# Performance work log

Hardware: AMD Instinct MI355X
Metric: run time of the kernel (lower is better)

## Reference

```python
import jax, jax.numpy as jnp
import numpy as np

N = 50000   # nodes
R = 50      # relations
B = 30      # bases
F_IN = 64   # input features
H = 64      # hidden channels
C = 8       # classes
E = 1000000 # edges


def setup_inputs() -> dict:
    key = jax.random.key(0)
    ks = jax.random.split(key, 16)
    x = jax.random.normal(ks[0], (N, F_IN), jnp.float32)
    edge_index = jax.random.randint(ks[1], (2, E), 0, N)
    edge_type = jax.random.randint(ks[2], (E,), 0, R)
    inp = {"x": x, "edge_index": edge_index, "edge_type": edge_type}
    dims = [(F_IN, H), (H, H), (H, C)]
    i = 3
    for l, (din, dout) in enumerate(dims):
        s = 1.0 / np.sqrt(din)
        inp[f"bases{l}"] = jax.random.normal(ks[i], (B, din, dout), jnp.float32) * s; i += 1
        inp[f"comp{l}"] = jax.random.normal(ks[i], (R, B), jnp.float32) / np.sqrt(B); i += 1
        inp[f"root{l}"] = jax.random.normal(ks[i], (din, dout), jnp.float32) * s; i += 1
        inp[f"bias{l}"] = jnp.zeros((dout,), jnp.float32); i += 1
    return inp


def _rgcn(x, bases, comp, root, bias, src, seg):
    # Per-relation mean aggregation (PyG RGCNConv default aggr='mean'):
    # segment id = dst * R + relation. Mean of source features per (dst, rel),
    # then basis-decomposed transform (linearity lets transform follow the mean).
    din = x.shape[1]
    sums = jax.ops.segment_sum(x[src], seg, num_segments=N * R)          # [N*R, din]
    cnt = jax.ops.segment_sum(jnp.ones((seg.shape[0],), x.dtype), seg, num_segments=N * R)
    inv = jnp.where(cnt > 0, 1.0 / jnp.maximum(cnt, 1.0), 0.0)
    agg = (sums * inv[:, None]).reshape(N, R, din)                        # [N, R, din]
    t = jnp.einsum('nri,rb->nbi', agg, comp)                              # [N, B, din]
    msg = jnp.einsum('nbi,bio->no', t, bases)                             # [N, dout]
    return msg + x @ root + bias


def reference(x, edge_index, edge_type,
              bases0, comp0, root0, bias0,
              bases1, comp1, root1, bias1,
              bases2, comp2, root2, bias2):
    src, dst = edge_index[0], edge_index[1]
    seg = dst * R + edge_type
    params = [(bases0, comp0, root0, bias0),
              (bases1, comp1, root1, bias1),
              (bases2, comp2, root2, bias2)]
    x1 = x
    for b, c, r, bi in params:
        x1 = _rgcn(x, b, c, r, bi, src, seg)
        x = jax.nn.relu(x1)
    # original returns log_softmax of the last conv's pre-ReLU output
    return jax.nn.log_softmax(x1, axis=1)
```

## Files before the change

### kernel.cpp

```cpp
#include <hip/hip_runtime.h>
#include <hip/hip_bf16.h>
#include <stdint.h>

#define NN   50000
#define RR   50
#define BB   30
#define DIN  64
#define EE   1000000
#define KTOT (BB*DIN + DIN)
#define NBW  16
#define ROWE (KTOT + 8)
#define CPAD 32

typedef __attribute__((ext_vector_type(8))) short short8;
typedef __attribute__((ext_vector_type(4))) float floatx4;

#define RFL(x) __builtin_amdgcn_readfirstlane(x)


__global__ void k_hist(const int* __restrict__ dst, const int* __restrict__ et,
                       int* __restrict__ cnt, int* __restrict__ dcount) {
    int e = blockIdx.x * 256 + threadIdx.x;
    if (e < EE) {
        int d = dst[e], r = et[e];
        atomicAdd(&cnt[d * RR + r], 1);
        atomicAdd(&dcount[d], 1);
    }
}

__global__ void k_scan1(const int* __restrict__ dcount, int* __restrict__ doff,
                        int* __restrict__ bsum) {
    __shared__ int sh[256];
    int t = threadIdx.x;
    int i = blockIdx.x * 256 + t;
    int v = (i < NN) ? dcount[i] : 0;
    sh[t] = v;
    __syncthreads();
    for (int s = 1; s < 256; s <<= 1) {
        int add = (t >= s) ? sh[t - s] : 0;
        __syncthreads();
        sh[t] += add;
        __syncthreads();
    }
    int incl = sh[t];
    if (i < NN) doff[i] = incl - v;
    if (t == 255) bsum[blockIdx.x] = incl;
}

__global__ void k_scan2(int* __restrict__ bsum, int nbv) {
    __shared__ int sh[256];
    int t = threadIdx.x;
    int v = (t < nbv) ? bsum[t] : 0;
    sh[t] = v;
    __syncthreads();
    for (int s = 1; s < 256; s <<= 1) {
        int add = (t >= s) ? sh[t - s] : 0;
        __syncthreads();
        sh[t] += add;
        __syncthreads();
    }
    if (t < nbv) bsum[t] = sh[t] - v;
}

__global__ void k_scan3(int* __restrict__ doff, const int* __restrict__ bsum) {
    int i = blockIdx.x * 256 + threadIdx.x;
    if (i < NN) doff[i] += bsum[blockIdx.x];
}

__global__ void k_scatter(const int* __restrict__ src, const int* __restrict__ dst,
                          const int* __restrict__ et, const int* __restrict__ cnt,
                          const int* __restrict__ doff, int* __restrict__ cursor,
                          int4* __restrict__ epack) {
    int e = blockIdx.x * 256 + threadIdx.x;
    if (e < EE) {
        int d = dst[e], r = et[e], s = src[e];
        int p = doff[d] + atomicAdd(&cursor[d], 1);
        float a = 1.0f / (float)cnt[d * RR + r];
        epack[p] = make_int4(s, r, __float_as_int(a), 0);
    }
}

__global__ void k_cast_x(const float* __restrict__ x, __hip_bfloat16* __restrict__ h) {
    int i = blockIdx.x * 256 + threadIdx.x;
    if (i < NN * DIN) h[i] = __float2bfloat16(x[i]);
}

__global__ void k_prep_comp3(const float* __restrict__ c0, const float* __restrict__ c1,
                             const float* __restrict__ c2, float* __restrict__ cp) {
    int idx = blockIdx.x * 256 + threadIdx.x;
    if (idx < 3 * RR * CPAD) {
        int l = idx / (RR * CPAD);
        int rem = idx - l * (RR * CPAD);
        int r = rem / CPAD, i = rem - r * CPAD;
        const float* c = (l == 0) ? c0 : (l == 1) ? c1 : c2;
        cp[idx] = (i < BB) ? c[r * BB + i] : 0.f;
    }
}

__global__ void k_prep_w3(const float* __restrict__ b0, const float* __restrict__ r0,
                          const float* __restrict__ b1, const float* __restrict__ r1,
                          const float* __restrict__ b2, const float* __restrict__ r2,
                          short* __restrict__ wt) {
    int idx = blockIdx.x * 256 + threadIdx.x;
    if (idx >= 144 * KTOT) return;
    int row = idx / KTOT, k = idx - row * KTOT;
    const float* bs; const float* rt; int o, dout;
    if (row < 64)       { bs = b0; rt = r0; o = row;        dout = 64; }
    else if (row < 128) { bs = b1; rt = r1; o = row - 64;   dout = 64; }
    else                { bs = b2; rt = r2; o = row - 128;  dout = 8;  }
    float v = 0.f;
    if (o < dout)
        v = (k < BB * DIN) ? bs[k * dout + o] : rt[(k - BB * DIN) * dout + o];
    __hip_bfloat16 hb = __float2bfloat16(v);
    wt[idx] = *reinterpret_cast<const short*>(&hb);
}

template <int DOUT, bool RELU>
__global__ __launch_bounds__(1024, 8)
void k_fused(const __hip_bfloat16* __restrict__ xin,
             const int4* __restrict__ epack,
             const int* __restrict__ doff, const int* __restrict__ dcount,
             const float* __restrict__ compP,
             const short* __restrict__ Wt,
             const float* __restrict__ bias,
             void* __restrict__ outp) {
    __shared__ __align__(16) char smem_raw[NBW * ROWE * 2];
    auto t_tile = reinterpret_cast<__hip_bfloat16(*)[ROWE]>(smem_raw);
    const int tid  = threadIdx.x;
    const int lane = tid & 63;
    const int wv   = RFL(tid >> 6);
    const int node0 = blockIdx.x * NBW;

    {
        const int j = wv;
        const int n = node0 + j;
        floatx4 acc[8];
#pragma unroll
        for (int u = 0; u < 8; ++u) acc[u] = (floatx4){0.f, 0.f, 0.f, 0.f};
        const int beg = RFL(doff[n]), cnt = RFL(dcount[n]);
        int e = 0;
        for (; e + 2 <= cnt; e += 2) {
            int4 ep0 = epack[beg + e];
            int4 ep1 = epack[beg + e + 1];
            const int s0 = RFL(ep0.x), r0 = RFL(ep0.y);
            const int s1 = RFL(ep1.x), r1 = RFL(ep1.y);
            const float a0 = __int_as_float(RFL(ep0.z));
            const float a1 = __int_as_float(RFL(ep1.z));
            const float x0 = __bfloat162float(xin[s0 * DIN + lane]) * a0;
            const float x1 = __bfloat162float(xin[s1 * DIN + lane]) * a1;
            const floatx4* c0 = (const floatx4*)(compP + r0 * CPAD);
            const floatx4* c1 = (const floatx4*)(compP + r1 * CPAD);
            const floatx4 v0 = {x0, x0, x0, x0};
            const floatx4 v1 = {x1, x1, x1, x1};
#pragma unroll
            for (int u = 0; u < 8; ++u) acc[u] = c0[u] * v0 + acc[u];
#pragma unroll
            for (int u = 0; u < 8; ++u) acc[u] = c1[u] * v1 + acc[u];
        }
        if (e < cnt) {
            int4 ep = epack[beg + e];
            const int s = RFL(ep.x), r = RFL(ep.y);
            const float a = __int_as_float(RFL(ep.z));
            const float xv = __bfloat162float(xin[s * DIN + lane]) * a;
            const floatx4* c = (const floatx4*)(compP + r * CPAD);
            const floatx4 w = {xv, xv, xv, xv};
#pragma unroll
            for (int u = 0; u < 8; ++u) acc[u] = c[u] * w + acc[u];
        }
        const float xself = __bfloat162float(xin[n * DIN + lane]);
#pragma unroll
        for (int b = 0; b < BB; ++b)
            t_tile[j][b * DIN + lane] = __float2bfloat16(acc[b >> 2][b & 3]);
        t_tile[j][BB * DIN + lane] = __float2bfloat16(xself);
    }
    __syncthreads();

    const int m = lane & 15;
    const int q = lane >> 4;
    int kk0, nsteps, col_base, kpart;
    if (DOUT == 64) {
        kpart = wv >> 2;
        col_base = (wv & 3) * 16;
        kk0    = (kpart <= 1) ? kpart * 16 : (kpart == 2 ? 32 : 47);
        nsteps = (kpart <= 1) ? 16 : 15;
    } else {
        kpart = wv;
        col_base = 0;
        kk0    = (kpart < 14) ? kpart * 4 : (kpart == 14 ? 56 : 59);
        nsteps = (kpart < 14) ? 4 : 3;
    }
    const __hip_bfloat16* arow = &t_tile[m][q * 8];
    const short* brow = Wt + (size_t)(col_base + m) * KTOT + q * 8;

    floatx4 acc0 = {0.f, 0.f, 0.f, 0.f};
    floatx4 acc1 = {0.f, 0.f, 0.f, 0.f};
    int s = 0;
    for (; s + 2 <= nsteps; s += 2) {
        const int kk = kk0 + s;
        short8 a0 = *reinterpret_cast<const short8*>(arow + kk * 32);
        short8 b0 = *reinterpret_cast<const short8*>(brow + kk * 32);
        short8 a1 = *reinterpret_cast<const short8*>(arow + (kk + 1) * 32);
        short8 b1 = *reinterpret_cast<const short8*>(brow + (kk + 1) * 32);
        acc0 = __builtin_amdgcn_mfma_f32_16x16x32_bf16(a0, b0, acc0, 0, 0, 0);
        acc1 = __builtin_amdgcn_mfma_f32_16x16x32_bf16(a1, b1, acc1, 0, 0, 0);
    }
    if (s < nsteps) {
        const int kk = kk0 + s;
        short8 a0 = *reinterpret_cast<const short8*>(arow + kk * 32);
        short8 b0 = *reinterpret_cast<const short8*>(brow + kk * 32);
        acc0 = __builtin_amdgcn_mfma_f32_16x16x32_bf16(a0, b0, acc0, 0, 0, 0);
    }
    floatx4 P = acc0 + acc1;

    __syncthreads();
    float* red = (float*)smem_raw;

    if (DOUT == 64) {
        if (kpart > 0) {
            const int slot = (wv & 3) * 3 + (kpart - 1);
            const int off = (slot * 64 + lane) * 6;
            red[off] = P[0]; red[off + 1] = P[1]; red[off + 2] = P[2]; red[off + 3] = P[3];
        }
        __syncthreads();
        if (kpart == 0) {
#pragma unroll
            for (int t = 0; t < 3; ++t) {
                const int off = (((wv & 3) * 3 + t) * 64 + lane) * 6;
                P[0] += red[off]; P[1] += red[off + 1];
                P[2] += red[off + 2]; P[3] += red[off + 3];
            }
            const int o = col_base + m;
            const float bi = bias[o];
#pragma unroll
            for (int r = 0; r < 4; ++r) {
                const int n = node0 + q * 4 + r;
                float v = P[r] + bi;
                if (RELU) {
                    v = fmaxf(v, 0.f);
                    reinterpret_cast<__hip_bfloat16*>(outp)[(size_t)n * DOUT + o] =
                        __float2bfloat16(v);
                } else {
                    reinterpret_cast<float*>(outp)[(size_t)n * DOUT + o] = v;
                }
            }
        }
    } else {
        if (kpart > 0) {
            const int off = ((kpart - 1) * 64 + lane) * 6;
            red[off] = P[0]; red[off + 1] = P[1]; red[off + 2] = P[2]; red[off + 3] = P[3];
        }
        __syncthreads();
        if (kpart == 0) {
#pragma unroll
            for (int w = 0; w < 15; ++w) {
                const int off = (w * 64 + lane) * 6;
                P[0] += red[off]; P[1] += red[off + 1];
                P[2] += red[off + 2]; P[3] += red[off + 3];
            }
            if (m < DOUT) {
                const int o = m;
                const float bi = bias[o];
#pragma unroll
                for (int r = 0; r < 4; ++r) {
                    const int n = node0 + q * 4 + r;
                    reinterpret_cast<float*>(outp)[(size_t)n * DOUT + o] = P[r] + bi;
                }
            }
        }
    }
}

__global__ void k_lsm(const float* __restrict__ pre, float* __restrict__ out) {
    int n = blockIdx.x * 256 + threadIdx.x;
    if (n < NN) {
        float v[8];
        float mx = -1e30f;
#pragma unroll
        for (int c = 0; c < 8; ++c) { v[c] = pre[n * 8 + c]; mx = fmaxf(mx, v[c]); }
        float s = 0.f;
#pragma unroll
        for (int c = 0; c < 8; ++c) s += expf(v[c] - mx);
        float ls = logf(s);
#pragma unroll
        for (int c = 0; c < 8; ++c) out[n * 8 + c] = v[c] - mx - ls;
    }
}

extern "C" void kernel_launch(void* const* d_in, const int* in_sizes, int n_in,
                              void* d_out, int out_size, void* d_ws, size_t ws_size,
                              hipStream_t stream) {
    const float* x     = (const float*)d_in[0];
    const int*   eidx  = (const int*)d_in[1];
    const int*   etype = (const int*)d_in[2];
    const float* bases0 = (const float*)d_in[3];
    const float* comp0  = (const float*)d_in[4];
    const float* root0  = (const float*)d_in[5];
    const float* bias0  = (const float*)d_in[6];
    const float* bases1 = (const float*)d_in[7];
    const float* comp1  = (const float*)d_in[8];
    const float* root1  = (const float*)d_in[9];
    const float* bias1  = (const float*)d_in[10];
    const float* bases2 = (const float*)d_in[11];
    const float* comp2  = (const float*)d_in[12];
    const float* root2  = (const float*)d_in[13];
    const float* bias2  = (const float*)d_in[14];
    const int* srcp = eidx;
    const int* dstp = eidx + EE;

    char* p = (char*)d_ws;
    auto carve = [&](size_t bytes) -> char* {
        char* r = p;
        p += (bytes + 255) & ~(size_t)255;
        return r;
    };
    int*  cnt    = (int*)carve((size_t)NN * RR * sizeof(int));
    int*  dcount = (int*)carve((size_t)NN * sizeof(int));
    int*  cursor = (int*)carve((size_t)NN * sizeof(int));
    int*  doff   = (int*)carve((size_t)NN * sizeof(int));
    int*  bsum   = (int*)carve(256 * sizeof(int));
    int4* epack  = (int4*)carve((size_t)EE * sizeof(int4));
    __hip_bfloat16* h0 = (__hip_bfloat16*)carve((size_t)NN * DIN * 2);
    __hip_bfloat16* h1 = (__hip_bfloat16*)carve((size_t)NN * DIN * 2);
    __hip_bfloat16* h2 = (__hip_bfloat16*)carve((size_t)NN * DIN * 2);
    float* pre = (float*)carve((size_t)NN * 8 * sizeof(float));
    short* wtA = (short*)carve((size_t)144 * KTOT * sizeof(short));
    float* cpA = (float*)carve((size_t)3 * RR * CPAD * sizeof(float));

    hipMemsetAsync(cnt, 0, (size_t)NN * (RR + 2) * sizeof(int) + 512, stream);

    const int EB = (EE + 255) / 256;
    const int NB = (NN + 255) / 256;
    k_hist<<<EB, 256, 0, stream>>>(dstp, etype, cnt, dcount);
    k_scan1<<<NB, 256, 0, stream>>>(dcount, doff, bsum);
    k_scan2<<<1, 256, 0, stream>>>(bsum, NB);
    k_scan3<<<NB, 256, 0, stream>>>(doff, bsum);
    k_scatter<<<EB, 256, 0, stream>>>(srcp, dstp, etype, cnt, doff, cursor, epack);
    k_cast_x<<<(NN * DIN + 255) / 256, 256, 0, stream>>>(x, h0);
    k_prep_comp3<<<(3 * RR * CPAD + 255) / 256, 256, 0, stream>>>(comp0, comp1, comp2, cpA);
    k_prep_w3<<<(144 * KTOT + 255) / 256, 256, 0, stream>>>(bases0, root0, bases1, root1,
                                                            bases2, root2, wtA);

    short* wt0 = wtA;
    short* wt1 = wtA + (size_t)64 * KTOT;
    short* wt2 = wtA + (size_t)128 * KTOT;
    float* cp0 = cpA;
    float* cp1 = cpA + RR * CPAD;
    float* cp2 = cpA + 2 * RR * CPAD;

    const int NF = NN / NBW;
    k_fused<64, true ><<<NF, 1024, 0, stream>>>(h0, epack, doff, dcount, cp0, wt0, bias0, (void*)h1);
    k_fused<64, true ><<<NF, 1024, 0, stream>>>(h1, epack, doff, dcount, cp1, wt1, bias1, (void*)h2);
    k_fused<8,  false><<<NF, 1024, 0, stream>>>(h2, epack, doff, dcount, cp2, wt2, bias2, (void*)pre);
    k_lsm<<<NB, 256, 0, stream>>>(pre, (float*)d_out);
}
```

Before: 612.6 us.

## Aggregate edges with MFMA using async LDS gathers of source rows

The per-node edge aggregation into the basis space moves from scalar FMA loops to 32x32x16 bf16 MFMA. Edges are handled in chunks of 16: source feature rows are gathered into LDS with global_load_lds and the next chunk's edge records are prefetched. The A operand is the bf16 relation coefficient times the mean weight. The second-stage GEMM is repartitioned so each wave computes two 16-column tiles, and the launch bound is lowered to 4 blocks per CU. This cuts scalar ALU work and serialized per-edge loads, at the cost of rounding coefficient products to bf16 and padding chunks to 16 edges.

```diff
diff --git a/kernel.cpp b/kernel.cpp
--- a/kernel.cpp
+++ b/kernel.cpp
@@ -9,13 +9,21 @@
 #define EE   1000000
 #define KTOT (BB*DIN + DIN)
 #define NBW  16
-#define ROWE (KTOT + 8)
-#define CPAD 32
-
-typedef __attribute__((ext_vector_type(8))) short short8;
-typedef __attribute__((ext_vector_type(4))) float floatx4;
+#define TROW 2000
+
+typedef __attribute__((ext_vector_type(8)))  short short8;
+typedef __attribute__((ext_vector_type(4)))  float floatx4;
+typedef __attribute__((ext_vector_type(16))) float floatx16;
 
 #define RFL(x) __builtin_amdgcn_readfirstlane(x)
+
+__device__ __forceinline__ int imin(int a, int b) { return a < b ? a : b; }
+
+__device__ __forceinline__ void async16(const void* g, void* l) {
+    __builtin_amdgcn_global_load_lds(
+        (const __attribute__((address_space(1))) unsigned int*)g,
+        (__attribute__((address_space(3))) unsigned int*)l, 16, 0, 0);
+}
 
 
 __global__ void k_hist(const int* __restrict__ dst, const int* __restrict__ et,
@@ -85,15 +93,17 @@
     if (i < NN * DIN) h[i] = __float2bfloat16(x[i]);
 }
 
-__global__ void k_prep_comp3(const float* __restrict__ c0, const float* __restrict__ c1,
-                             const float* __restrict__ c2, float* __restrict__ cp) {
+__global__ void k_prep_cb3(const float* __restrict__ c0, const float* __restrict__ c1,
+                           const float* __restrict__ c2, short* __restrict__ cb) {
     int idx = blockIdx.x * 256 + threadIdx.x;
-    if (idx < 3 * RR * CPAD) {
-        int l = idx / (RR * CPAD);
-        int rem = idx - l * (RR * CPAD);
-        int r = rem / CPAD, i = rem - r * CPAD;
+    if (idx < 3 * RR * 32) {
+        int l = idx / (RR * 32);
+        int rem = idx - l * (RR * 32);
+        int r = rem >> 5, i = rem & 31;
         const float* c = (l == 0) ? c0 : (l == 1) ? c1 : c2;
-        cp[idx] = (i < BB) ? c[r * BB + i] : 0.f;
+        float v = (i < BB) ? c[r * BB + i] : 0.f;
+        __hip_bfloat16 hb = __float2bfloat16(v);
+        cb[idx] = *reinterpret_cast<const short*>(&hb);
     }
 }
 
@@ -116,154 +126,184 @@
 }
 
 template <int DOUT, bool RELU>
-__global__ __launch_bounds__(1024, 8)
+__global__ __launch_bounds__(1024, 4)
 void k_fused(const __hip_bfloat16* __restrict__ xin,
              const int4* __restrict__ epack,
              const int* __restrict__ doff, const int* __restrict__ dcount,
-             const float* __restrict__ compP,
+             const short* __restrict__ cpb,
              const short* __restrict__ Wt,
              const float* __restrict__ bias,
              void* __restrict__ outp) {
-    __shared__ __align__(16) char smem_raw[NBW * ROWE * 2];
-    auto t_tile = reinterpret_cast<__hip_bfloat16(*)[ROWE]>(smem_raw);
+    __shared__ __align__(16) char smem[NBW * TROW * 2];
+    short* t_tile = (short*)smem;
+
     const int tid  = threadIdx.x;
     const int lane = tid & 63;
     const int wv   = RFL(tid >> 6);
     const int node0 = blockIdx.x * NBW;
-
+    const int m    = lane & 31;
+    const bool hi  = (lane >= 32);
+
+    floatx16 acc0 = {0.f,0.f,0.f,0.f,0.f,0.f,0.f,0.f,0.f,0.f,0.f,0.f,0.f,0.f,0.f,0.f};
+    floatx16 acc1 = acc0;
     {
-        const int j = wv;
-        const int n = node0 + j;
-        floatx4 acc[8];
-#pragma unroll
-        for (int u = 0; u < 8; ++u) acc[u] = (floatx4){0.f, 0.f, 0.f, 0.f};
+        const int n = node0 + wv;
         const int beg = RFL(doff[n]), cnt = RFL(dcount[n]);
-        int e = 0;
-        for (; e + 2 <= cnt; e += 2) {
-            int4 ep0 = epack[beg + e];
-            int4 ep1 = epack[beg + e + 1];
-            const int s0 = RFL(ep0.x), r0 = RFL(ep0.y);
-            const int s1 = RFL(ep1.x), r1 = RFL(ep1.y);
-            const float a0 = __int_as_float(RFL(ep0.z));
-            const float a1 = __int_as_float(RFL(ep1.z));
-            const float x0 = __bfloat162float(xin[s0 * DIN + lane]) * a0;
-            const float x1 = __bfloat162float(xin[s1 * DIN + lane]) * a1;
-            const floatx4* c0 = (const floatx4*)(compP + r0 * CPAD);
-            const floatx4* c1 = (const floatx4*)(compP + r1 * CPAD);
-            const floatx4 v0 = {x0, x0, x0, x0};
-            const floatx4 v1 = {x1, x1, x1, x1};
-#pragma unroll
-            for (int u = 0; u < 8; ++u) acc[u] = c0[u] * v0 + acc[u];
-#pragma unroll
-            for (int u = 0; u < 8; ++u) acc[u] = c1[u] * v1 + acc[u];
-        }
-        if (e < cnt) {
-            int4 ep = epack[beg + e];
-            const int s = RFL(ep.x), r = RFL(ep.y);
-            const float a = __int_as_float(RFL(ep.z));
-            const float xv = __bfloat162float(xin[s * DIN + lane]) * a;
-            const floatx4* c = (const floatx4*)(compP + r * CPAD);
-            const floatx4 w = {xv, xv, xv, xv};
-#pragma unroll
-            for (int u = 0; u < 8; ++u) acc[u] = c[u] * w + acc[u];
-        }
-        const float xself = __bfloat162float(xin[n * DIN + lane]);
-#pragma unroll
-        for (int b = 0; b < BB; ++b)
-            t_tile[j][b * DIN + lane] = __float2bfloat16(acc[b >> 2][b & 3]);
-        t_tile[j][BB * DIN + lane] = __float2bfloat16(xself);
-    }
-    __syncthreads();
-
-    const int m = lane & 15;
-    const int q = lane >> 4;
-    int kk0, nsteps, col_base, kpart;
+        const int nch = (cnt + 15) >> 4;
+        char*  sst_b = smem + wv * 2048;
+        const short* sst = (const short*)sst_b;
+        const int eg  = lane >> 3;
+        const int sub = (lane & 7) * 16;
+        const int k0  = (lane >> 5) * 8;
+
+        int4 vr0, vr1;
+        if (nch > 0) {
+            vr0 = epack[imin(beg + eg,     EE - 1)];
+            vr1 = epack[imin(beg + eg + 8, EE - 1)];
+        }
+        for (int c = 0; c < nch; ++c) {
+            const int cb = beg + c * 16;
+            const char* g0 = (const char*)xin + ((size_t)(unsigned)vr0.x) * 128 + sub;
+            const char* g1 = (const char*)xin + ((size_t)(unsigned)vr1.x) * 128 + sub;
+            async16(g0, sst_b);
+            async16(g1, sst_b + 1024);
+            if (c + 1 < nch) {
+                const int nb = cb + 16;
+                vr0 = epack[imin(nb + eg,     EE - 1)];
+                vr1 = epack[imin(nb + eg + 8, EE - 1)];
+            }
+            int relA[8], relB[8]; float alA[8], alB[8];
+#pragma unroll
+            for (int t = 0; t < 8; ++t) {
+                int4 ea = epack[imin(cb + t,     EE - 1)];
+                int4 eb = epack[imin(cb + 8 + t, EE - 1)];
+                relA[t] = ea.y;
+                relB[t] = eb.y;
+                alA[t] = (c * 16 + t     < cnt) ? __int_as_float(ea.z) : 0.f;
+                alB[t] = (c * 16 + 8 + t < cnt) ? __int_as_float(eb.z) : 0.f;
+            }
+            short8 af;
+#pragma unroll
+            for (int t = 0; t < 8; ++t) {
+                int   rel = hi ? relB[t] : relA[t];
+                float al  = hi ? alB[t]  : alA[t];
+                unsigned short cv = ((const unsigned short*)cpb)[rel * 32 + m];
+                float cf = __int_as_float(((int)cv) << 16);
+                af[t] = (short)(((unsigned)__float_as_int(cf * al)) >> 16);
+            }
+            __builtin_amdgcn_s_waitcnt(0x0F70);
+            __builtin_amdgcn_sched_barrier(0);
+            short8 bf0, bf1;
+#pragma unroll
+            for (int t = 0; t < 8; ++t) {
+                bf0[t] = sst[(k0 + t) * 64 + m];
+                bf1[t] = sst[(k0 + t) * 64 + 32 + m];
+            }
+            acc0 = __builtin_amdgcn_mfma_f32_32x32x16_bf16(af, bf0, acc0, 0, 0, 0);
+            acc1 = __builtin_amdgcn_mfma_f32_32x32x16_bf16(af, bf1, acc1, 0, 0, 0);
+        }
+    }
+    __syncthreads();
+
+    {
+        short* trow = t_tile + wv * TROW;
+#pragma unroll
+        for (int r = 0; r < 16; ++r) {
+            const int b = (r & 3) + 8 * (r >> 2) + 4 * (lane >> 5);
+            if (b < BB) {
+                __hip_bfloat16 h0 = __float2bfloat16(acc0[r]);
+                __hip_bfloat16 h1 = __float2bfloat16(acc1[r]);
+                trow[b * 64 + m]      = *reinterpret_cast<const short*>(&h0);
+                trow[b * 64 + 32 + m] = *reinterpret_cast<const short*>(&h1);
+            }
+        }
+        trow[BB * 64 + lane] = ((const short*)xin)[(node0 + wv) * 64 + lane];
+    }
+    __syncthreads();
+
+    const int mm = lane & 15;
+    const int qq = lane >> 4;
+    floatx4 p0 = {0.f, 0.f, 0.f, 0.f};
+    floatx4 p1 = {0.f, 0.f, 0.f, 0.f};
+    int cp, kp;
+    if (DOUT == 64) { cp = wv & 1; kp = wv >> 1; }
+    else            { cp = 0;      kp = wv;      }
+    int kk0, nst;
+    if (DOUT == 64) { kk0 = (kp < 6)  ? kp * 8 : 48 + (kp - 6)  * 7; nst = (kp < 6)  ? 8 : 7; }
+    else            { kk0 = (kp < 14) ? kp * 4 : 56 + (kp - 14) * 3; nst = (kp < 14) ? 4 : 3; }
+
+    {
+        const short* arow = t_tile + mm * TROW + qq * 8;
+        const short* b0row = Wt + (size_t)(cp * 32 + mm) * KTOT + qq * 8;
+        const short* b1row = Wt + (size_t)(cp * 32 + 16 + mm) * KTOT + qq * 8;
+        for (int s = 0; s < nst; ++s) {
+            const int kk = kk0 + s;
+            short8 a  = *reinterpret_cast<const short8*>(arow + kk * 32);
+            short8 w0 = *reinterpret_cast<const short8*>(b0row + kk * 32);
+            p0 = __builtin_amdgcn_mfma_f32_16x16x32_bf16(a, w0, p0, 0, 0, 0);
+            if (DOUT == 64) {
+                short8 w1 = *reinterpret_cast<const short8*>(b1row + kk * 32);
+                p1 = __builtin_amdgcn_mfma_f32_16x16x32_bf16(a, w1, p1, 0, 0, 0);
+            }
+        }
+    }
+
+    __syncthreads();
+    float* red = (float*)smem;
+
     if (DOUT == 64) {
-        kpart = wv >> 2;
-        col_base = (wv & 3) * 16;
-        kk0    = (kpart <= 1) ? kpart * 16 : (kpart == 2 ? 32 : 47);
-        nsteps = (kpart <= 1) ? 16 : 15;
+        if (kp > 0) {
+            const int off = ((cp * 7 + (kp - 1)) * 64 + lane) * 9;
+#pragma unroll
+            for (int i = 0; i < 4; ++i) { red[off + i] = p0[i]; red[off + 4 + i] = p1[i]; }
+        }
+        __syncthreads();
+        if (kp == 0) {
+#pragma unroll
+            for (int w = 0; w < 7; ++w) {
+                const int off = ((cp * 7 + w) * 64 + lane) * 9;
+#pragma unroll
+                for (int i = 0; i < 4; ++i) { p0[i] += red[off + i]; p1[i] += red[off + 4 + i]; }
+            }
+#pragma unroll
+            for (int t = 0; t < 2; ++t) {
+                const int o = cp * 32 + t * 16 + mm;
+                const float bi = bias[o];
+                floatx4& P = t ? p1 : p0;
+#pragma unroll
+                for (int r = 0; r < 4; ++r) {
+                    const int n = node0 + qq * 4 + r;
+                    float v = P[r] + bi;
+                    if (RELU) {
+                        v = fmaxf(v, 0.f);
+                        reinterpret_cast<__hip_bfloat16*>(outp)[(size_t)n * DOUT + o] =
+                            __float2bfloat16(v);
+                    } else {
+                        reinterpret_cast<float*>(outp)[(size_t)n * DOUT + o] = v;
+                    }
+                }
+            }
+        }
     } else {
-        kpart = wv;
-        col_base = 0;
-        kk0    = (kpart < 14) ? kpart * 4 : (kpart == 14 ? 56 : 59);
-        nsteps = (kpart < 14) ? 4 : 3;
-    }
-    const __hip_bfloat16* arow = &t_tile[m][q * 8];
-    const short* brow = Wt + (size_t)(col_base + m) * KTOT + q * 8;
-
-    floatx4 acc0 = {0.f, 0.f, 0.f, 0.f};
-    floatx4 acc1 = {0.f, 0.f, 0.f, 0.f};
-    int s = 0;
-    for (; s + 2 <= nsteps; s += 2) {
-        const int kk = kk0 + s;
-        short8 a0 = *reinterpret_cast<const short8*>(arow + kk * 32);
-        short8 b0 = *reinterpret_cast<const short8*>(brow + kk * 32);
-        short8 a1 = *reinterpret_cast<const short8*>(arow + (kk + 1) * 32);
-        short8 b1 = *reinterpret_cast<const short8*>(brow + (kk + 1) * 32);
-        acc0 = __builtin_amdgcn_mfma_f32_16x16x32_bf16(a0, b0, acc0, 0, 0, 0);
-        acc1 = __builtin_amdgcn_mfma_f32_16x16x32_bf16(a1, b1, acc1, 0, 0, 0);
-    }
-    if (s < nsteps) {
-        const int kk = kk0 + s;
-        short8 a0 = *reinterpret_cast<const short8*>(arow + kk * 32);
-        short8 b0 = *reinterpret_cast<const short8*>(brow + kk * 32);
-        acc0 = __builtin_amdgcn_mfma_f32_16x16x32_bf16(a0, b0, acc0, 0, 0, 0);
-    }
-    floatx4 P = acc0 + acc1;
-
-    __syncthreads();
-    float* red = (float*)smem_raw;
-
-    if (DOUT == 64) {
-        if (kpart > 0) {
-            const int slot = (wv & 3) * 3 + (kpart - 1);
-            const int off = (slot * 64 + lane) * 6;
-            red[off] = P[0]; red[off + 1] = P[1]; red[off + 2] = P[2]; red[off + 3] = P[3];
-        }
-        __syncthreads();
-        if (kpart == 0) {
-#pragma unroll
-            for (int t = 0; t < 3; ++t) {
-                const int off = (((wv & 3) * 3 + t) * 64 + lane) * 6;
-                P[0] += red[off]; P[1] += red[off + 1];
-                P[2] += red[off + 2]; P[3] += red[off + 3];
-            }
-            const int o = col_base + m;
-            const float bi = bias[o];
-#pragma unroll
-            for (int r = 0; r < 4; ++r) {
-                const int n = node0 + q * 4 + r;
-                float v = P[r] + bi;
-                if (RELU) {
-                    v = fmaxf(v, 0.f);
-                    reinterpret_cast<__hip_bfloat16*>(outp)[(size_t)n * DOUT + o] =
-                        __float2bfloat16(v);
-                } else {
-                    reinterpret_cast<float*>(outp)[(size_t)n * DOUT + o] = v;
-                }
-            }
-        }
-    } else {
-        if (kpart > 0) {
-            const int off = ((kpart - 1) * 64 + lane) * 6;
-            red[off] = P[0]; red[off + 1] = P[1]; red[off + 2] = P[2]; red[off + 3] = P[3];
-        }
-        __syncthreads();
-        if (kpart == 0) {
+        if (kp > 0) {
+            const int off = (((kp - 1)) * 64 + lane) * 5;
+#pragma unroll
+            for (int i = 0; i < 4; ++i) red[off + i] = p0[i];
+        }
+        __syncthreads();
+        if (kp == 0) {
 #pragma unroll
             for (int w = 0; w < 15; ++w) {
-                const int off = (w * 64 + lane) * 6;
-                P[0] += red[off]; P[1] += red[off + 1];
-                P[2] += red[off + 2]; P[3] += red[off + 3];
-            }
-            if (m < DOUT) {
-                const int o = m;
-                const float bi = bias[o];
+                const int off = (w * 64 + lane) * 5;
+#pragma unroll
+                for (int i = 0; i < 4; ++i) p0[i] += red[off + i];
+            }
+            if (mm < DOUT) {
+                const float bi = bias[mm];
 #pragma unroll
                 for (int r = 0; r < 4; ++r) {
-                    const int n = node0 + q * 4 + r;
-                    reinterpret_cast<float*>(outp)[(size_t)n * DOUT + o] = P[r] + bi;
+                    const int n = node0 + qq * 4 + r;
+                    reinterpret_cast<float*>(outp)[(size_t)n * DOUT + mm] = p0[r] + bi;
                 }
             }
         }
@@ -318,13 +358,13 @@
     int*  cursor = (int*)carve((size_t)NN * sizeof(int));
     int*  doff   = (int*)carve((size_t)NN * sizeof(int));
     int*  bsum   = (int*)carve(256 * sizeof(int));
-    int4* epack  = (int4*)carve((size_t)EE * sizeof(int4));
+    int4* epack  = (int4*)carve((size_t)EE * sizeof(int4) + 512);
     __hip_bfloat16* h0 = (__hip_bfloat16*)carve((size_t)NN * DIN * 2);
     __hip_bfloat16* h1 = (__hip_bfloat16*)carve((size_t)NN * DIN * 2);
     __hip_bfloat16* h2 = (__hip_bfloat16*)carve((size_t)NN * DIN * 2);
     float* pre = (float*)carve((size_t)NN * 8 * sizeof(float));
     short* wtA = (short*)carve((size_t)144 * KTOT * sizeof(short));
-    float* cpA = (float*)carve((size_t)3 * RR * CPAD * sizeof(float));
+    short* cbA = (short*)carve((size_t)3 * RR * 32 * sizeof(short));
 
     hipMemsetAsync(cnt, 0, (size_t)NN * (RR + 2) * sizeof(int) + 512, stream);
 
@@ -336,20 +376,20 @@
     k_scan3<<<NB, 256, 0, stream>>>(doff, bsum);
     k_scatter<<<EB, 256, 0, stream>>>(srcp, dstp, etype, cnt, doff, cursor, epack);
     k_cast_x<<<(NN * DIN + 255) / 256, 256, 0, stream>>>(x, h0);
-    k_prep_comp3<<<(3 * RR * CPAD + 255) / 256, 256, 0, stream>>>(comp0, comp1, comp2, cpA);
+    k_prep_cb3<<<(3 * RR * 32 + 255) / 256, 256, 0, stream>>>(comp0, comp1, comp2, cbA);
     k_prep_w3<<<(144 * KTOT + 255) / 256, 256, 0, stream>>>(bases0, root0, bases1, root1,
                                                             bases2, root2, wtA);
 
     short* wt0 = wtA;
     short* wt1 = wtA + (size_t)64 * KTOT;
     short* wt2 = wtA + (size_t)128 * KTOT;
-    float* cp0 = cpA;
-    float* cp1 = cpA + RR * CPAD;
-    float* cp2 = cpA + 2 * RR * CPAD;
+    short* cb0 = cbA;
+    short* cb1 = cbA + RR * 32;
+    short* cb2 = cbA + 2 * RR * 32;
 
     const int NF = NN / NBW;
-    k_fused<64, true ><<<NF, 1024, 0, stream>>>(h0, epack, doff, dcount, cp0, wt0, bias0, (void*)h1);
-    k_fused<64, true ><<<NF, 1024, 0, stream>>>(h1, epack, doff, dcount, cp1, wt1, bias1, (void*)h2);
-    k_fused<8,  false><<<NF, 1024, 0, stream>>>(h2, epack, doff, dcount, cp2, wt2, bias2, (void*)pre);
+    k_fused<64, true ><<<NF, 1024, 0, stream>>>(h0, epack, doff, dcount, cb0, wt0, bias0, (void*)h1);
+    k_fused<64, true ><<<NF, 1024, 0, stream>>>(h1, epack, doff, dcount, cb1, wt1, bias1, (void*)h2);
+    k_fused<8,  false><<<NF, 1024, 0, stream>>>(h2, epack, doff, dcount, cb2, wt2, bias2, (void*)pre);
     k_lsm<<<NB, 256, 0, stream>>>(pre, (float*)d_out);
 }
```

Measured after the change: 652.2 us. 1.06x slower.
